# Performance work log

Measured on AMD Instinct MI355X. Metric: run time of the kernel, lower is better.

## Reference

```python
import jax, jax.numpy as jnp
import numpy as np
from jax import lax

V, H, A, S = 256, 2048, 512, 512  # vocab, hidden, attn, seq_len


def setup_inputs() -> dict:
    key = jax.random.key(0)
    ks = jax.random.split(key, 8)
    sc = 0.02  # small init to keep tanh unsaturated
    return {
        "x_enc": jax.random.normal(ks[0], (S, V), jnp.float32),
        "x_dec": jax.random.normal(ks[1], (S, V), jnp.float32),
        "W_enc": jax.random.normal(ks[2], (H, V + H), jnp.float32) * sc,
        "b_enc": jnp.zeros((H,), jnp.float32),
        "Wa_enc": jax.random.normal(ks[3], (A, H), jnp.float32) * sc,
        "Wa_dec": jax.random.normal(ks[4], (A, H), jnp.float32) * sc,
        "v_a": jax.random.normal(ks[5], (A,), jnp.float32) * sc,
        "W_dec": jax.random.normal(ks[6], (H, V + 2 * H), jnp.float32) * sc,
        "b_dec": jnp.zeros((H,), jnp.float32),
        "W_out": jax.random.normal(ks[7], (V, H), jnp.float32) * sc,
        "b_out": jnp.zeros((V,), jnp.float32),
    }


def reference(x_enc, x_dec, W_enc, b_enc, Wa_enc, Wa_dec, v_a, W_dec, b_dec, W_out, b_out):
    h0 = jnp.zeros((W_enc.shape[0],), x_enc.dtype)

    # Encoder: h_t = tanh(W_enc [x_t ; h_{t-1}] + b)
    def enc_step(h, x):
        h_new = jnp.tanh(jnp.concatenate([x, h]) @ W_enc.T + b_enc)
        return h_new, h_new

    h_enc, enc_states = lax.scan(enc_step, h0, x_enc)  # enc_states: (S, H)

    # Encoder-side attention projection is step-invariant -> hoist (same math).
    enc_proj = enc_states @ Wa_enc.T  # (S, A)

    # Decoder with per-step Bahdanau additive attention.
    def dec_step(h, x):
        dec_proj = h @ Wa_dec.T                              # (A,)
        energy = jnp.tanh(enc_proj + dec_proj) @ v_a         # (S,)
        attn_w = jax.nn.softmax(energy)                      # (S,)
        context = attn_w @ enc_states                        # (H,)
        h_new = jnp.tanh(jnp.concatenate([x, context, h]) @ W_dec.T + b_dec)
        logits = h_new @ W_out.T + b_out                     # (V,)
        return h_new, logits

    _, outputs = lax.scan(dec_step, h_enc, x_dec)  # (S, V)
    return outputs
```

## Files before the change

### kernel.cpp

```cpp
#include <hip/hip_runtime.h>

#define V 256
#define H 2048
#define A 512
#define S 512
#define NBLK 128
#define NTHR 512
#define CH 64
#define HPH (512*CH)
#define DPH (128*CH)
#define SENTU 0x7FC00000u
#define SENT64 0x7FC000007FC00000ULL

typedef float f32x4 __attribute__((ext_vector_type(4)));
typedef float f32x2 __attribute__((ext_vector_type(2)));
typedef unsigned long long u64;

__device__ __forceinline__ f32x4 ld_cg4(const float* p) {
    f32x4 r;
    asm volatile("global_load_dwordx4 %0, %1, off sc0 sc1\n\ts_waitcnt vmcnt(0)"
                 : "=&v"(r) : "v"(p) : "memory");
    return r;
}
__device__ __forceinline__ f32x4 poll4(const float* p) {
    f32x4 r = ld_cg4(p);
    while (__float_as_uint(r.x) == SENTU || __float_as_uint(r.y) == SENTU ||
           __float_as_uint(r.z) == SENTU || __float_as_uint(r.w) == SENTU)
        r = ld_cg4(p);
    return r;
}

__device__ __forceinline__ void st_pub2(float* p, float x, float y) {
    f32x2 v; v.x = x; v.y = y;
    asm volatile("s_waitcnt vmcnt(0)\n\tglobal_store_dwordx2 %0, %1, off sc0 sc1"
                 :: "v"(p), "v"(v) : "memory");
}
__device__ __forceinline__ void st_pub1(float* p, float x) {
    asm volatile("s_waitcnt vmcnt(0)\n\tglobal_store_dword %0, %1, off sc0 sc1"
                 :: "v"(p), "v"(x) : "memory");
}
__device__ __forceinline__ void vm_drain() { asm volatile("s_waitcnt vmcnt(0)" ::: "memory"); }
__device__ __forceinline__ void ax_st64(u64* p, u64 v) {
    (void)__hip_atomic_exchange(p, v, __ATOMIC_RELAXED, __HIP_MEMORY_SCOPE_AGENT);
}
__device__ __forceinline__ u64 pack2(float a, float b) {
    return ((u64)__float_as_uint(b) << 32) | (u64)__float_as_uint(a);
}
__device__ __forceinline__ void st_rst2(float* p) {
    f32x2 v; v.x = __uint_as_float(SENTU); v.y = __uint_as_float(SENTU);
    asm volatile("global_store_dwordx2 %0, %1, off sc0 sc1" :: "v"(p), "v"(v) : "memory");
}
__device__ __forceinline__ void st_rst1(float* p) {
    float v = __uint_as_float(SENTU);
    asm volatile("global_store_dword %0, %1, off sc0 sc1" :: "v"(p), "v"(v) : "memory");
}

__global__ void init_ex(unsigned* p, int n) {
    int i = blockIdx.x * blockDim.x + threadIdx.x;
    if (i < n) p[i] = SENTU;
}

__global__ __launch_bounds__(256) void gemm_nt(
    const float* __restrict__ Amat, int lda,
    const float* __restrict__ Bmat, int ldb,
    float* __restrict__ C, int ldc,
    const float* __restrict__ bias, int M, int N, int K)
{
    __shared__ float As[16][68];
    __shared__ float Bs[16][68];
    const int tid = threadIdx.x;
    const int tx = tid & 15;
    const int ty = tid >> 4;
    const int m0 = blockIdx.y * 64;
    const int n0 = blockIdx.x * 64;
    const int lr = tid >> 2;
    const int lk = (tid & 3) * 4;

    float acc[4][4] = {};
    for (int k0 = 0; k0 < K; k0 += 16) {
        float4 av = *(const float4*)(Amat + (size_t)(m0 + lr) * lda + k0 + lk);
        float4 bv = *(const float4*)(Bmat + (size_t)(n0 + lr) * ldb + k0 + lk);
        __syncthreads();
        As[lk+0][lr] = av.x; As[lk+1][lr] = av.y; As[lk+2][lr] = av.z; As[lk+3][lr] = av.w;
        Bs[lk+0][lr] = bv.x; Bs[lk+1][lr] = bv.y; Bs[lk+2][lr] = bv.z; Bs[lk+3][lr] = bv.w;
        __syncthreads();
        #pragma unroll
        for (int k = 0; k < 16; ++k) {
            float a4[4], b4[4];
            #pragma unroll
            for (int i = 0; i < 4; ++i) a4[i] = As[k][ty*4+i];
            #pragma unroll
            for (int j = 0; j < 4; ++j) b4[j] = Bs[k][tx*4+j];
            #pragma unroll
            for (int i = 0; i < 4; ++i)
                #pragma unroll
                for (int j = 0; j < 4; ++j) acc[i][j] += a4[i] * b4[j];
        }
    }
    #pragma unroll
    for (int i = 0; i < 4; ++i) {
        const int m = m0 + ty*4 + i;
        #pragma unroll
        for (int j = 0; j < 4; ++j) {
            const int n = n0 + tx*4 + j;
            float v = acc[i][j];
            if (bias) v += bias[n];
            C[(size_t)m * ldc + n] = v;
        }
    }
}

__global__ __launch_bounds__(NTHR, 2) void enc_scan(
    const float* __restrict__ W_enc, const float* __restrict__ x_enc,
    const float* __restrict__ b_enc,
    float* __restrict__ states, float* __restrict__ hex)
{
    __shared__ __align__(16) float hs[2][H];
    __shared__ __align__(16) float xs[2][V];
    const int tid = threadIdx.x;
    const int wid = tid >> 6, lane = tid & 63;
    const int w   = blockIdx.x * 8 + wid;
    const int r0  = 2*w, r1 = r0 + 1;
    const int slot = (w >> 1)*CH + (w & 1)*2;

    f32x4 we0[8], we1[8];
    #pragma unroll
    for (int k = 0; k < 8; ++k) {
        we0[k] = *(const f32x4*)(W_enc + (size_t)r0*(V+H) + V + 4*(lane + 64*k));
        we1[k] = *(const f32x4*)(W_enc + (size_t)r1*(V+H) + V + 4*(lane + 64*k));
    }
    const f32x4 wx0 = *(const f32x4*)(W_enc + (size_t)r0*(V+H) + 4*lane);
    const f32x4 wx1 = *(const f32x4*)(W_enc + (size_t)r1*(V+H) + 4*lane);
    const float bb0 = b_enc[r0], bb1 = b_enc[r1];

    if (tid < 64) ((f32x4*)xs[0])[tid] = ((const f32x4*)x_enc)[tid];
    __syncthreads();
    {
        f32x4 xv = ((const f32x4*)xs[0])[lane];
        float a0 = wx0.x*xv.x + wx0.y*xv.y + wx0.z*xv.z + wx0.w*xv.w;
        float a1 = wx1.x*xv.x + wx1.y*xv.y + wx1.z*xv.z + wx1.w*xv.w;
        #pragma unroll
        for (int off = 32; off; off >>= 1) { a0 += __shfl_down(a0, off); a1 += __shfl_down(a1, off); }
        if (lane == 0) {
            float h0 = tanhf(a0 + bb0), h1 = tanhf(a1 + bb1);
            vm_drain();
            ax_st64((u64*)(hex + 0*HPH + slot), pack2(h0, h1));
            states[r0] = h0; states[r1] = h1;
        }
    }

    for (int t = 1; t < S; ++t) {
        if (tid < 64) ((f32x4*)xs[t&1])[tid] = ((const f32x4*)(x_enc + (size_t)t*V))[tid];
        ((f32x4*)hs[t&1])[tid] = poll4(hex + ((t-1)%3)*HPH + tid*CH);
        __syncthreads();
        if (lane == 0) st_rst2(hex + ((t+1)%3)*HPH + slot);

        f32x4 xv = ((const f32x4*)xs[t&1])[lane];
        float a0 = wx0.x*xv.x + wx0.y*xv.y + wx0.z*xv.z + wx0.w*xv.w;
        float a1 = wx1.x*xv.x + wx1.y*xv.y + wx1.z*xv.z + wx1.w*xv.w;
        const f32x4* h4 = (const f32x4*)hs[t&1];
        #pragma unroll
        for (int k = 0; k < 8; ++k) {
            f32x4 hv = h4[lane + 64*k];
            a0 += we0[k].x*hv.x + we0[k].y*hv.y + we0[k].z*hv.z + we0[k].w*hv.w;
            a1 += we1[k].x*hv.x + we1[k].y*hv.y + we1[k].z*hv.z + we1[k].w*hv.w;
        }
        #pragma unroll
        for (int off = 32; off; off >>= 1) { a0 += __shfl_down(a0, off); a1 += __shfl_down(a1, off); }
        if (lane == 0) {
            float h0 = tanhf(a0 + bb0), h1 = tanhf(a1 + bb1);
            vm_drain();
            ax_st64((u64*)(hex + (t%3)*HPH + slot), pack2(h0, h1));
            states[(size_t)t*H + r0] = h0;
            states[(size_t)t*H + r1] = h1;
        }
    }
}

__global__ __launch_bounds__(NTHR, 2) void dec_scan(
    const float* __restrict__ Wa_dec, const float* __restrict__ W_dec,
    const float* __restrict__ enc_proj, const float* __restrict__ v_a,
    const float* __restrict__ x_dec, const float* __restrict__ b_dec,
    const float* __restrict__ enc_states, float* __restrict__ h_dec,
    float* __restrict__ hexd, float* __restrict__ dpex, float* __restrict__ eex)
{
    __shared__ __align__(16) float hs[2][H];
    __shared__ __align__(16) float ps[A];
    __shared__ __align__(16) float es[S];
    __shared__ __align__(16) float xs[2][V];
    __shared__ __align__(16) float wct[8][2][S];
    __shared__ float zred[8];
    const int tid = threadIdx.x;
    const int wid = tid >> 6, lane = tid & 63;
    const int w   = blockIdx.x * 8 + wid;
    const int r0  = 2*w, r1 = r0 + 1;
    const int hslot = (w >> 1)*CH + (w & 1)*2;
    const bool attn = ((w & 1) == 0);
    const int s_row = w >> 1;
    const int aslot = (s_row >> 2)*CH + (s_row & 3);

    f32x4 wc0[2], wc1[2];
    {
        f32x4 wcr0[8], wcr1[8];
        #pragma unroll
        for (int k = 0; k < 8; ++k) {
            wcr0[k] = *(const f32x4*)(W_dec + (size_t)r0*(V+2*H) + V + 4*(lane + 64*k));
            wcr1[k] = *(const f32x4*)(W_dec + (size_t)r1*(V+2*H) + V + 4*(lane + 64*k));
        }
        for (int s = 0; s < S; ++s) {
            ((f32x4*)hs[s&1])[tid] = ((const f32x4*)(enc_states + (size_t)s*H))[tid];
            __syncthreads();
            const f32x4* h4 = (const f32x4*)hs[s&1];
            float p0 = 0.f, p1 = 0.f;
            #pragma unroll
            for (int k = 0; k < 8; ++k) {
                f32x4 hv = h4[lane + 64*k];
                p0 += wcr0[k].x*hv.x + wcr0[k].y*hv.y + wcr0[k].z*hv.z + wcr0[k].w*hv.w;
                p1 += wcr1[k].x*hv.x + wcr1[k].y*hv.y + wcr1[k].z*hv.z + wcr1[k].w*hv.w;
            }
            #pragma unroll
            for (int off = 32; off; off >>= 1) { p0 += __shfl_down(p0, off); p1 += __shfl_down(p1, off); }
            if (lane == 0) { wct[wid][0][s] = p0; wct[wid][1][s] = p1; }
        }
        __syncthreads();
        #pragma unroll
        for (int k = 0; k < 2; ++k) {
            wc0[k] = *(const f32x4*)(&wct[wid][0][4*(lane + 64*k)]);
            wc1[k] = *(const f32x4*)(&wct[wid][1][4*(lane + 64*k)]);
        }
        __syncthreads();
    }

    f32x4 wh0[8], wh1[8], wa[8], ep[2], va[2];
    #pragma unroll
    for (int k = 0; k < 8; ++k) {
        wh0[k] = *(const f32x4*)(W_dec + (size_t)r0*(V+2*H) + V + H + 4*(lane + 64*k));
        wh1[k] = *(const f32x4*)(W_dec + (size_t)r1*(V+2*H) + V + H + 4*(lane + 64*k));
        wa[k]  = (f32x4)(0.f);
    }
    #pragma unroll
    for (int k = 0; k < 2; ++k) { ep[k] = (f32x4)(0.f); va[k] = (f32x4)(0.f); }
    if (attn) {
        #pragma unroll
        for (int k = 0; k < 8; ++k)
            wa[k] = *(const f32x4*)(Wa_dec + (size_t)s_row*H + 4*(lane + 64*k));
        #pragma unroll
        for (int k = 0; k < 2; ++k) {
            ep[k] = *(const f32x4*)(enc_proj + (size_t)s_row*A + 4*(lane + 64*k));
            va[k] = *(const f32x4*)(v_a + 4*(lane + 64*k));
        }
    }
    const f32x4 wx0 = *(const f32x4*)(W_dec + (size_t)r0*(V+2*H) + 4*lane);
    const f32x4 wx1 = *(const f32x4*)(W_dec + (size_t)r1*(V+2*H) + 4*lane);
    const float bb0 = b_dec[r0], bb1 = b_dec[r1];

    const f32x4* ps4 = (const f32x4*)ps;
    const f32x4* es4 = (const f32x4*)es;

    for (int t = 0; t < S; ++t) {
        const int ph  = t % 3;
        const int phn = (t+1) % 3;
        const int php = (t+2) % 3;

        if (tid < 64) ((f32x4*)xs[t&1])[tid] = ((const f32x4*)(x_dec + (size_t)t*V))[tid];

        if (t == 0) ((f32x4*)hs[0])[tid] = ((const f32x4*)(enc_states + (size_t)(S-1)*H))[tid];
        else        ((f32x4*)hs[t&1])[tid] = poll4(hexd + php*HPH + tid*CH);
        __syncthreads();

        if (lane == 0) st_rst2(hexd + phn*HPH + hslot);
        if (t > 0 && attn && lane == 0) {
            st_rst1(dpex + php*DPH + aslot);
            st_rst1(eex  + php*DPH + aslot);
        }

        const f32x4* h4 = (const f32x4*)hs[t&1];

        if (attn) {
            float aP = 0.f;
            #pragma unroll
            for (int k = 0; k < 8; ++k) {
                f32x4 hv = h4[lane + 64*k];
                aP += wa[k].x*hv.x + wa[k].y*hv.y + wa[k].z*hv.z + wa[k].w*hv.w;
            }
            #pragma unroll
            for (int off = 32; off; off >>= 1) aP += __shfl_down(aP, off);
            if (lane == 0) st_pub1(dpex + ph*DPH + aslot, aP);
        }
        f32x4 xv = ((const f32x4*)xs[t&1])[lane];
        float aH0 = wx0.x*xv.x + wx0.y*xv.y + wx0.z*xv.z + wx0.w*xv.w;
        float aH1 = wx1.x*xv.x + wx1.y*xv.y + wx1.z*xv.z + wx1.w*xv.w;
        #pragma unroll
        for (int k = 0; k < 8; ++k) {
            f32x4 hv = h4[lane + 64*k];
            aH0 += wh0[k].x*hv.x + wh0[k].y*hv.y + wh0[k].z*hv.z + wh0[k].w*hv.w;
            aH1 += wh1[k].x*hv.x + wh1[k].y*hv.y + wh1[k].z*hv.z + wh1[k].w*hv.w;
        }
        #pragma unroll
        for (int off = 32; off; off >>= 1) { aH0 += __shfl_down(aH0, off); aH1 += __shfl_down(aH1, off); }

        if (tid < 128) ((f32x4*)ps)[tid] = poll4(dpex + ph*DPH + tid*CH);
        __syncthreads();
        if (attn) {
            float e_ = 0.f;
            #pragma unroll
            for (int k = 0; k < 2; ++k) {
                f32x4 p = ps4[lane + 64*k];
                e_ += va[k].x*tanhf(ep[k].x + p.x) + va[k].y*tanhf(ep[k].y + p.y)
                    + va[k].z*tanhf(ep[k].z + p.z) + va[k].w*tanhf(ep[k].w + p.w);
            }
            #pragma unroll
            for (int off = 32; off; off >>= 1) e_ += __shfl_down(e_, off);
            if (lane == 0) st_pub1(eex + ph*DPH + aslot, expf(e_));
        }

        if (tid < 128) ((f32x4*)es)[tid] = poll4(eex + ph*DPH + tid*CH);
        __syncthreads();

        float z = es[tid];
        #pragma unroll
        for (int off = 32; off; off >>= 1) z += __shfl_down(z, off);
        if (lane == 0) zred[wid] = z;
        __syncthreads();
        const float Z = zred[0]+zred[1]+zred[2]+zred[3]+zred[4]+zred[5]+zred[6]+zred[7];

        float c0 = 0.f, c1 = 0.f;
        #pragma unroll
        for (int k = 0; k < 2; ++k) {
            f32x4 ev = es4[lane + 64*k];
            c0 += wc0[k].x*ev.x + wc0[k].y*ev.y + wc0[k].z*ev.z + wc0[k].w*ev.w;
            c1 += wc1[k].x*ev.x + wc1[k].y*ev.y + wc1[k].z*ev.z + wc1[k].w*ev.w;
        }
        #pragma unroll
        for (int off = 32; off; off >>= 1) { c0 += __shfl_down(c0, off); c1 += __shfl_down(c1, off); }

        if (lane == 0) {
            const float Zi = 1.f / Z;
            float h0 = tanhf(aH0 + bb0 + c0*Zi);
            float h1 = tanhf(aH1 + bb1 + c1*Zi);
            st_pub2(hexd + ph*HPH + hslot, h0, h1);
            f32x2 hv; hv.x = h0; hv.y = h1;
            *(f32x2*)(h_dec + (size_t)t*H + r0) = hv;
        }
    }
}

extern "C" void kernel_launch(void* const* d_in, const int* in_sizes, int n_in,
                              void* d_out, int out_size, void* d_ws, size_t ws_size,
                              hipStream_t stream) {
    const float* x_enc  = (const float*)d_in[0];
    const float* x_dec  = (const float*)d_in[1];
    const float* W_enc  = (const float*)d_in[2];
    const float* b_enc  = (const float*)d_in[3];
    const float* Wa_enc = (const float*)d_in[4];
    const float* Wa_dec = (const float*)d_in[5];
    const float* v_a    = (const float*)d_in[6];
    const float* W_dec  = (const float*)d_in[7];
    const float* b_dec  = (const float*)d_in[8];
    const float* W_out  = (const float*)d_in[9];
    const float* b_out  = (const float*)d_in[10];
    float* out = (float*)d_out;

    float* ws         = (float*)d_ws;
    float* enc_states = ws;
    float* enc_proj   = enc_states + (size_t)S*H;
    float* h_dec      = enc_proj + (size_t)S*A;
    float* hex_e      = h_dec + (size_t)S*H;
    float* hex_d      = hex_e + 3*HPH;
    float* dp_ex      = hex_d + 3*HPH;
    float* e_ex       = dp_ex + 3*DPH;
    const int n_ex = 3*HPH*2 + 3*DPH*2;

    dim3 b256(256);

    init_ex<<<dim3((n_ex + 255)/256), b256, 0, stream>>>((unsigned*)hex_e, n_ex);

    {
        const float* We = W_enc; const float* xe = x_enc; const float* be = b_enc;
        float* st = enc_states; float* hx = hex_e;
        void* args[] = { &We, &xe, &be, &st, &hx };
        hipLaunchCooperativeKernel((void*)enc_scan, dim3(NBLK), dim3(NTHR), args, 0, stream);
    }

    gemm_nt<<<dim3(A/64, S/64), b256, 0, stream>>>(enc_states, H, Wa_enc, H, enc_proj, A, nullptr, S, A, H);

    {
        const float* wa = Wa_dec; const float* wd = W_dec; const float* epj = enc_proj;
        const float* vv = v_a; const float* xd = x_dec; const float* bd = b_dec;
        const float* est = enc_states; float* hd = h_dec;
        float* hx = hex_d; float* dx = dp_ex; float* ex = e_ex;
        void* args[] = { &wa, &wd, &epj, &vv, &xd, &bd, &est, &hd, &hx, &dx, &ex };
        hipLaunchCooperativeKernel((void*)dec_scan, dim3(NBLK), dim3(NTHR), args, 0, stream);
    }

    gemm_nt<<<dim3(V/64, S/64), b256, 0, stream>>>(h_dec, H, W_out, H, out, V, b_out, S, V, H);
}
```

Before: 6.387 ms.

## Fuse attention projection and energy into producer blocks; precompute W_c·enc_states via GEMM

```diff
diff --git a/kernel.cpp b/kernel.cpp
--- a/kernel.cpp
+++ b/kernel.cpp
@@ -5,12 +5,12 @@
 #define A 512
 #define S 512
 #define NBLK 128
+#define NPROD 32
 #define NTHR 512
 #define CH 64
 #define HPH (512*CH)
-#define DPH (128*CH)
+#define PPH (128*128)
 #define SENTU 0x7FC00000u
-#define SENT64 0x7FC000007FC00000ULL
 
 typedef float f32x4 __attribute__((ext_vector_type(4)));
 typedef float f32x2 __attribute__((ext_vector_type(2)));
@@ -29,15 +29,41 @@
         r = ld_cg4(p);
     return r;
 }
-
+__device__ __forceinline__ bool anynan(f32x4 v) {
+    return __float_as_uint(v.x) == SENTU || __float_as_uint(v.y) == SENTU ||
+           __float_as_uint(v.z) == SENTU || __float_as_uint(v.w) == SENTU;
+}
+__device__ __forceinline__ void poll8(const float* p, f32x4 o[8]) {
+    for (;;) {
+        f32x4 a0,a1,a2,a3,a4,a5,a6,a7;
+        asm volatile(
+            "global_load_dwordx4 %0, %8, off sc0 sc1\n\t"
+            "global_load_dwordx4 %1, %8, off offset:16 sc0 sc1\n\t"
+            "global_load_dwordx4 %2, %8, off offset:32 sc0 sc1\n\t"
+            "global_load_dwordx4 %3, %8, off offset:48 sc0 sc1\n\t"
+            "global_load_dwordx4 %4, %8, off offset:64 sc0 sc1\n\t"
+            "global_load_dwordx4 %5, %8, off offset:80 sc0 sc1\n\t"
+            "global_load_dwordx4 %6, %8, off offset:96 sc0 sc1\n\t"
+            "global_load_dwordx4 %7, %8, off offset:112 sc0 sc1\n\t"
+            "s_waitcnt vmcnt(0)"
+            : "=&v"(a0),"=&v"(a1),"=&v"(a2),"=&v"(a3),
+              "=&v"(a4),"=&v"(a5),"=&v"(a6),"=&v"(a7)
+            : "v"(p) : "memory");
+        if (!(anynan(a0)||anynan(a1)||anynan(a2)||anynan(a3)||
+              anynan(a4)||anynan(a5)||anynan(a6)||anynan(a7))) {
+            o[0]=a0;o[1]=a1;o[2]=a2;o[3]=a3;o[4]=a4;o[5]=a5;o[6]=a6;o[7]=a7;
+            return;
+        }
+    }
+}
 __device__ __forceinline__ void st_pub2(float* p, float x, float y) {
     f32x2 v; v.x = x; v.y = y;
     asm volatile("s_waitcnt vmcnt(0)\n\tglobal_store_dwordx2 %0, %1, off sc0 sc1"
                  :: "v"(p), "v"(v) : "memory");
 }
-__device__ __forceinline__ void st_pub1(float* p, float x) {
-    asm volatile("s_waitcnt vmcnt(0)\n\tglobal_store_dword %0, %1, off sc0 sc1"
-                 :: "v"(p), "v"(x) : "memory");
+__device__ __forceinline__ void st_pub4(float* p, f32x4 v) {
+    asm volatile("s_waitcnt vmcnt(0)\n\tglobal_store_dwordx4 %0, %1, off sc0 sc1"
+                 :: "v"(p), "v"(v) : "memory");
 }
 __device__ __forceinline__ void vm_drain() { asm volatile("s_waitcnt vmcnt(0)" ::: "memory"); }
 __device__ __forceinline__ void ax_st64(u64* p, u64 v) {
@@ -50,9 +76,9 @@
     f32x2 v; v.x = __uint_as_float(SENTU); v.y = __uint_as_float(SENTU);
     asm volatile("global_store_dwordx2 %0, %1, off sc0 sc1" :: "v"(p), "v"(v) : "memory");
 }
-__device__ __forceinline__ void st_rst1(float* p) {
-    float v = __uint_as_float(SENTU);
-    asm volatile("global_store_dword %0, %1, off sc0 sc1" :: "v"(p), "v"(v) : "memory");
+__device__ __forceinline__ void st_rst4(float* p) {
+    f32x4 v; v.x = v.y = v.z = v.w = __uint_as_float(SENTU);
+    asm volatile("global_store_dwordx4 %0, %1, off sc0 sc1" :: "v"(p), "v"(v) : "memory");
 }
 
 __global__ void init_ex(unsigned* p, int n) {
@@ -180,81 +206,51 @@
 __global__ __launch_bounds__(NTHR, 2) void dec_scan(
     const float* __restrict__ Wa_dec, const float* __restrict__ W_dec,
     const float* __restrict__ enc_proj, const float* __restrict__ v_a,
-    const float* __restrict__ x_dec, const float* __restrict__ b_dec,
+    const float* __restrict__ WcT, const float* __restrict__ x_dec,
+    const float* __restrict__ b_dec,
     const float* __restrict__ enc_states, float* __restrict__ h_dec,
-    float* __restrict__ hexd, float* __restrict__ dpex, float* __restrict__ eex)
+    float* __restrict__ hexd, float* __restrict__ peex)
 {
     __shared__ __align__(16) float hs[2][H];
-    __shared__ __align__(16) float ps[A];
     __shared__ __align__(16) float es[S];
     __shared__ __align__(16) float xs[2][V];
-    __shared__ __align__(16) float wct[8][2][S];
+    __shared__ __align__(16) float epT[16][S];
+    __shared__ __align__(16) float pel[S];
+    __shared__ __align__(16) f32x4 pl[4][128];
+    __shared__ float dpl[16];
+    __shared__ float vsm[16];
     __shared__ float zred[8];
     const int tid = threadIdx.x;
     const int wid = tid >> 6, lane = tid & 63;
-    const int w   = blockIdx.x * 8 + wid;
+    const int bid = blockIdx.x;
+    const int w   = bid * 8 + wid;
     const int r0  = 2*w, r1 = r0 + 1;
     const int hslot = (w >> 1)*CH + (w & 1)*2;
-    const bool attn = ((w & 1) == 0);
-    const int s_row = w >> 1;
-    const int aslot = (s_row >> 2)*CH + (s_row & 3);
-
-    f32x4 wc0[2], wc1[2];
-    {
-        f32x4 wcr0[8], wcr1[8];
-        #pragma unroll
-        for (int k = 0; k < 8; ++k) {
-            wcr0[k] = *(const f32x4*)(W_dec + (size_t)r0*(V+2*H) + V + 4*(lane + 64*k));
-            wcr1[k] = *(const f32x4*)(W_dec + (size_t)r1*(V+2*H) + V + 4*(lane + 64*k));
-        }
-        for (int s = 0; s < S; ++s) {
-            ((f32x4*)hs[s&1])[tid] = ((const f32x4*)(enc_states + (size_t)s*H))[tid];
-            __syncthreads();
-            const f32x4* h4 = (const f32x4*)hs[s&1];
-            float p0 = 0.f, p1 = 0.f;
-            #pragma unroll
-            for (int k = 0; k < 8; ++k) {
-                f32x4 hv = h4[lane + 64*k];
-                p0 += wcr0[k].x*hv.x + wcr0[k].y*hv.y + wcr0[k].z*hv.z + wcr0[k].w*hv.w;
-                p1 += wcr1[k].x*hv.x + wcr1[k].y*hv.y + wcr1[k].z*hv.z + wcr1[k].w*hv.w;
-            }
-            #pragma unroll
-            for (int off = 32; off; off >>= 1) { p0 += __shfl_down(p0, off); p1 += __shfl_down(p1, off); }
-            if (lane == 0) { wct[wid][0][s] = p0; wct[wid][1][s] = p1; }
-        }
-        __syncthreads();
-        #pragma unroll
-        for (int k = 0; k < 2; ++k) {
-            wc0[k] = *(const f32x4*)(&wct[wid][0][4*(lane + 64*k)]);
-            wc1[k] = *(const f32x4*)(&wct[wid][1][4*(lane + 64*k)]);
-        }
-        __syncthreads();
-    }
-
-    f32x4 wh0[8], wh1[8], wa[8], ep[2], va[2];
+    const bool prod = (bid < NPROD);
+    const int abase = bid * 16;
+
+    f32x4 wh0[8], wh1[8], wc0[2], wc1[2];
     #pragma unroll
     for (int k = 0; k < 8; ++k) {
         wh0[k] = *(const f32x4*)(W_dec + (size_t)r0*(V+2*H) + V + H + 4*(lane + 64*k));
         wh1[k] = *(const f32x4*)(W_dec + (size_t)r1*(V+2*H) + V + H + 4*(lane + 64*k));
-        wa[k]  = (f32x4)(0.f);
     }
     #pragma unroll
-    for (int k = 0; k < 2; ++k) { ep[k] = (f32x4)(0.f); va[k] = (f32x4)(0.f); }
-    if (attn) {
-        #pragma unroll
-        for (int k = 0; k < 8; ++k)
-            wa[k] = *(const f32x4*)(Wa_dec + (size_t)s_row*H + 4*(lane + 64*k));
-        #pragma unroll
-        for (int k = 0; k < 2; ++k) {
-            ep[k] = *(const f32x4*)(enc_proj + (size_t)s_row*A + 4*(lane + 64*k));
-            va[k] = *(const f32x4*)(v_a + 4*(lane + 64*k));
-        }
+    for (int k = 0; k < 2; ++k) {
+        wc0[k] = *(const f32x4*)(WcT + (size_t)r0*S + 4*(lane + 64*k));
+        wc1[k] = *(const f32x4*)(WcT + (size_t)r1*S + 4*(lane + 64*k));
     }
     const f32x4 wx0 = *(const f32x4*)(W_dec + (size_t)r0*(V+2*H) + 4*lane);
     const f32x4 wx1 = *(const f32x4*)(W_dec + (size_t)r1*(V+2*H) + 4*lane);
     const float bb0 = b_dec[r0], bb1 = b_dec[r1];
 
-    const f32x4* ps4 = (const f32x4*)ps;
+    if (prod) {
+        #pragma unroll
+        for (int al = 0; al < 16; ++al)
+            epT[al][tid] = enc_proj[(size_t)tid*A + abase + al];
+        if (tid < 16) vsm[tid] = v_a[abase + tid];
+    }
+
     const f32x4* es4 = (const f32x4*)es;
 
     for (int t = 0; t < S; ++t) {
@@ -269,24 +265,38 @@
         __syncthreads();
 
         if (lane == 0) st_rst2(hexd + phn*HPH + hslot);
-        if (t > 0 && attn && lane == 0) {
-            st_rst1(dpex + php*DPH + aslot);
-            st_rst1(eex  + php*DPH + aslot);
-        }
+        if (t > 0 && prod && tid < 128)
+            st_rst4(peex + php*PPH + tid*128 + bid*4);
 
         const f32x4* h4 = (const f32x4*)hs[t&1];
 
-        if (attn) {
-            float aP = 0.f;
+        if (prod) {
+            const size_t wbase = (size_t)(abase + 2*wid) * H;
+            float d0 = 0.f, d1 = 0.f;
             #pragma unroll
             for (int k = 0; k < 8; ++k) {
+                f32x4 a0 = *(const f32x4*)(Wa_dec + wbase + 4*(lane + 64*k));
+                f32x4 a1 = *(const f32x4*)(Wa_dec + wbase + H + 4*(lane + 64*k));
                 f32x4 hv = h4[lane + 64*k];
-                aP += wa[k].x*hv.x + wa[k].y*hv.y + wa[k].z*hv.z + wa[k].w*hv.w;
+                d0 += a0.x*hv.x + a0.y*hv.y + a0.z*hv.z + a0.w*hv.w;
+                d1 += a1.x*hv.x + a1.y*hv.y + a1.z*hv.z + a1.w*hv.w;
             }
             #pragma unroll
-            for (int off = 32; off; off >>= 1) aP += __shfl_down(aP, off);
-            if (lane == 0) st_pub1(dpex + ph*DPH + aslot, aP);
-        }
+            for (int off = 32; off; off >>= 1) { d0 += __shfl_down(d0, off); d1 += __shfl_down(d1, off); }
+            if (lane == 0) { dpl[2*wid] = d0; dpl[2*wid+1] = d1; }
+            __syncthreads();
+            float pe = 0.f;
+            #pragma unroll
+            for (int al = 0; al < 16; ++al)
+                pe += vsm[al] * tanhf(epT[al][tid] + dpl[al]);
+            pel[tid] = pe;
+            __syncthreads();
+            if (tid < 128) {
+                f32x4 v = *(const f32x4*)(&pel[4*tid]);
+                st_pub4(peex + ph*PPH + tid*128 + bid*4, v);
+            }
+        }
+
         f32x4 xv = ((const f32x4*)xs[t&1])[lane];
         float aH0 = wx0.x*xv.x + wx0.y*xv.y + wx0.z*xv.z + wx0.w*xv.w;
         float aH1 = wx1.x*xv.x + wx1.y*xv.y + wx1.z*xv.z + wx1.w*xv.w;
@@ -299,22 +309,20 @@
         #pragma unroll
         for (int off = 32; off; off >>= 1) { aH0 += __shfl_down(aH0, off); aH1 += __shfl_down(aH1, off); }
 
-        if (tid < 128) ((f32x4*)ps)[tid] = poll4(dpex + ph*DPH + tid*CH);
-        __syncthreads();
-        if (attn) {
-            float e_ = 0.f;
-            #pragma unroll
-            for (int k = 0; k < 2; ++k) {
-                f32x4 p = ps4[lane + 64*k];
-                e_ += va[k].x*tanhf(ep[k].x + p.x) + va[k].y*tanhf(ep[k].y + p.y)
-                    + va[k].z*tanhf(ep[k].z + p.z) + va[k].w*tanhf(ep[k].w + p.w);
-            }
-            #pragma unroll
-            for (int off = 32; off; off >>= 1) e_ += __shfl_down(e_, off);
-            if (lane == 0) st_pub1(eex + ph*DPH + aslot, expf(e_));
-        }
-
-        if (tid < 128) ((f32x4*)es)[tid] = poll4(eex + ph*DPH + tid*CH);
+        {
+            const int g = tid >> 7, c = tid & 127;
+            f32x4 o[8];
+            poll8(peex + ph*PPH + c*128 + g*32, o);
+            pl[g][c] = (o[0]+o[1]) + (o[2]+o[3]) + ((o[4]+o[5]) + (o[6]+o[7]));
+        }
+        __syncthreads();
+        if (tid < 128) {
+            f32x4 tot = (pl[0][tid] + pl[1][tid]) + (pl[2][tid] + pl[3][tid]);
+            es[4*tid+0] = expf(tot.x);
+            es[4*tid+1] = expf(tot.y);
+            es[4*tid+2] = expf(tot.z);
+            es[4*tid+3] = expf(tot.w);
+        }
         __syncthreads();
 
         float z = es[tid];
@@ -364,12 +372,12 @@
     float* ws         = (float*)d_ws;
     float* enc_states = ws;
     float* enc_proj   = enc_states + (size_t)S*H;
-    float* h_dec      = enc_proj + (size_t)S*A;
+    float* WcT        = enc_proj + (size_t)S*A;
+    float* h_dec      = WcT + (size_t)H*S;
     float* hex_e      = h_dec + (size_t)S*H;
     float* hex_d      = hex_e + 3*HPH;
-    float* dp_ex      = hex_d + 3*HPH;
-    float* e_ex       = dp_ex + 3*DPH;
-    const int n_ex = 3*HPH*2 + 3*DPH*2;
+    float* pe_ex      = hex_d + 3*HPH;
+    const int n_ex = 3*HPH*2 + 3*PPH;
 
     dim3 b256(256);
 
@@ -383,13 +391,14 @@
     }
 
     gemm_nt<<<dim3(A/64, S/64), b256, 0, stream>>>(enc_states, H, Wa_enc, H, enc_proj, A, nullptr, S, A, H);
+    gemm_nt<<<dim3(S/64, H/64), b256, 0, stream>>>(W_dec + V, V+2*H, enc_states, H, WcT, S, nullptr, H, S, H);
 
     {
         const float* wa = Wa_dec; const float* wd = W_dec; const float* epj = enc_proj;
-        const float* vv = v_a; const float* xd = x_dec; const float* bd = b_dec;
-        const float* est = enc_states; float* hd = h_dec;
-        float* hx = hex_d; float* dx = dp_ex; float* ex = e_ex;
-        void* args[] = { &wa, &wd, &epj, &vv, &xd, &bd, &est, &hd, &hx, &dx, &ex };
+        const float* vv = v_a; const float* wc = WcT; const float* xd = x_dec;
+        const float* bd = b_dec; const float* est = enc_states; float* hd = h_dec;
+        float* hx = hex_d; float* px = pe_ex;
+        void* args[] = { &wa, &wd, &epj, &vv, &wc, &xd, &bd, &est, &hd, &hx, &px };
         hipLaunchCooperativeKernel((void*)dec_scan, dim3(NBLK), dim3(NTHR), args, 0, stream);
     }
 
```

Result: slower. 9.121 ms (+42.8%).
